# Optimization experiments

Hardware: AMD Instinct MI355X
Metric: run time of the kernel (lower is better)

## Reference

```python
import jax, jax.numpy as jnp
import numpy as np

K_SLOTS = 64
DIM = 256
HEADS = 4
DH = DIM // HEADS
EPS = 1e-20
LN_EPS = 1e-5


def layernorm(x, g, b):
    mu = jnp.mean(x, axis=-1, keepdims=True)
    var = jnp.var(x, axis=-1, keepdims=True)
    return (x - mu) * jax.lax.rsqrt(var + LN_EPS) * g + b


def setup_inputs() -> dict:
    key = jax.random.key(0)
    ks = jax.random.split(key, 12)
    B, S = 4, 32768
    s = 0.02
    return {
        "X": jax.random.normal(ks[0], (B, S, DIM), dtype=jnp.float32),
        "mu": jax.random.uniform(ks[1], (1, K_SLOTS, DIM), minval=-0.2, maxval=0.2, dtype=jnp.float32),
        "ln_s_g": jnp.ones((DIM,), jnp.float32),
        "ln_s_b": jnp.zeros((DIM,), jnp.float32),
        "Wq": jax.random.normal(ks[2], (DIM, DIM), jnp.float32) * s,
        "bq": jax.random.normal(ks[3], (DIM,), jnp.float32) * s,
        "Wk": jax.random.normal(ks[4], (DIM, DIM), jnp.float32) * s,
        "bk": jax.random.normal(ks[5], (DIM,), jnp.float32) * s,
        "Wv": jax.random.normal(ks[6], (DIM, DIM), jnp.float32) * s,
        "bv": jax.random.normal(ks[7], (DIM,), jnp.float32) * s,
        "ln_a_g": jnp.ones((DIM,), jnp.float32),
        "ln_a_b": jnp.zeros((DIM,), jnp.float32),
    }


def reference(X, mu, ln_s_g, ln_s_b, Wq, bq, Wk, bk, Wv, bv, ln_a_g, ln_a_b):
    B, S, D = X.shape
    # slots (eval mode: mu is used directly), LN then q projection
    Sq = layernorm(mu, ln_s_g, ln_s_b) @ Wq + bq            # [1, K, D]
    Q = Sq.reshape(K_SLOTS, HEADS, DH)                       # [K, H, dh] (shared over batch)
    Kp = (X @ Wk + bk).reshape(B, S, HEADS, DH)              # [B, S, H, dh]
    V = (X @ Wv + bv).reshape(B, S, HEADS, DH)
    scale = 1.0 / np.sqrt(DH).astype(np.float32)
    # scores [B, H, K, S]
    W = jnp.einsum("khd,bshd->bhks", Q, Kp) * scale
    # softmax over SLOT axis (k), then sum-normalize over sequence axis (s)
    W = jax.nn.softmax(W, axis=2)
    C = jnp.sum(W, axis=-1, keepdims=True)                   # [B, H, K, 1]
    A = W / (C + EPS)
    S_hat = jnp.einsum("bhks,bshd->bkhd", A, V).reshape(B, K_SLOTS, D)
    return layernorm(S_hat, ln_a_g, ln_a_b)
```

## Files before the change

### kernel.cpp

```cpp
#include <hip/hip_runtime.h>
#include <hip/hip_bf16.h>

#define DIM   256
#define DH    64
#define NKS   64
#define NH    4
#define SEQ   32768
#define NCOPY 8

typedef float f32x4  __attribute__((ext_vector_type(4)));
typedef short bf16x8 __attribute__((ext_vector_type(8)));

__device__ __forceinline__ unsigned short f2bf(float f) {
    union { __hip_bfloat16 b; unsigned short u; } v;
    v.b = __float2bfloat16(f);
    return v.u;
}
__device__ __forceinline__ unsigned int f2bf2(float lo, float hi) {
    return (unsigned int)f2bf(lo) | ((unsigned int)f2bf(hi) << 16);
}

__global__ void k_q(const float* __restrict__ mu, const float* __restrict__ g,
                    const float* __restrict__ bb, const float* __restrict__ Wq,
                    const float* __restrict__ bq, float* __restrict__ Q) {
    __shared__ float nrm[DIM];
    __shared__ float red1[4], red2[4];
    const int k = blockIdx.x, t = threadIdx.x;
    float x = mu[k * DIM + t];
    float s = x;
    #pragma unroll
    for (int o = 1; o <= 32; o <<= 1) s += __shfl_xor(s, o);
    if ((t & 63) == 0) red1[t >> 6] = s;
    __syncthreads();
    const float mean = (red1[0] + red1[1] + red1[2] + red1[3]) * (1.0f / DIM);
    const float d = x - mean;
    float vs = d * d;
    #pragma unroll
    for (int o = 1; o <= 32; o <<= 1) vs += __shfl_xor(vs, o);
    if ((t & 63) == 0) red2[t >> 6] = vs;
    __syncthreads();
    const float var = (red2[0] + red2[1] + red2[2] + red2[3]) * (1.0f / DIM);
    nrm[t] = d * rsqrtf(var + 1e-5f) * g[t] + bb[t];
    __syncthreads();
    float acc = bq[t];
    for (int c = 0; c < DIM; ++c) acc += nrm[c] * Wq[c * DIM + t];
    Q[k * DIM + t] = acc;
}

__global__ void k_fold(const float* __restrict__ Q, const float* __restrict__ Wk,
                       const float* __restrict__ bk, const float* __restrict__ Wv,
                       const float* __restrict__ bv,
                       unsigned short* __restrict__ W2T, float* __restrict__ b2) {
    const int n = blockIdx.x, t = threadIdx.x;
    __shared__ float q[DH];
    if (n < 256) {
        const int h = n >> 6, k = n & 63;
        if (t < DH) q[t] = Q[k * DIM + h * DH + t];
        __syncthreads();
        float acc = 0.f;
        #pragma unroll 8
        for (int d0 = 0; d0 < DH; ++d0) acc += Wk[t * DIM + h * DH + d0] * q[d0];
        W2T[n * 256 + t] = f2bf(acc * 0.125f);
        if (t == 0) {
            float ba = 0.f;
            for (int d0 = 0; d0 < DH; ++d0) ba += bk[h * DH + d0] * q[d0];
            b2[n] = ba * 0.125f;
        }
    } else {
        const int col = n - 256;
        W2T[n * 256 + t] = f2bf(Wv[t * DIM + col]);
        if (t == 0) b2[n] = bv[col];
    }
}

__global__ __launch_bounds__(1024)
void k_main_part(const float* __restrict__ X, const unsigned short* __restrict__ W2T,
                 const float* __restrict__ b2, float* __restrict__ num_p,
                 float* __restrict__ den_p) {
    extern __shared__ __align__(16) unsigned char smem[];
    const int AB = 32768, VB = 49152, SB = 65536;
    const int tid  = threadIdx.x;
    const int lane = tid & 63;
    const int wid  = tid >> 6;
    const int l15  = lane & 15;
    const int lhi  = lane >> 4;
    const int bid   = blockIdx.x;
    const int b     = bid >> 6;
    const int chunk = bid & 63;
    const float* Xg = X + ((size_t)(b * SEQ + chunk * 512)) * DIM;

    const bool is_score = wid < 8;
    const int h_sc  = wid >> 1;
    const int sh    = wid & 1;
    const int vg    = wid - 8;
    const int h_v   = vg >> 1;
    const int nbase = wid * 32;
    const int hp = wid >> 2;
    const int dq = wid & 3;

    bf16x8 bfr[8][2];
    #pragma unroll
    for (int ks = 0; ks < 8; ++ks)
        #pragma unroll
        for (int ni = 0; ni < 2; ++ni)
            bfr[ks][ni] = *(const bf16x8*)(W2T + (size_t)(nbase + ni * 16 + l15) * 256
                                           + ks * 32 + lhi * 8);
    float bias[2];
    #pragma unroll
    for (int ni = 0; ni < 2; ++ni) bias[ni] = b2[nbase + ni * 16 + l15];

    f32x4 pv[4];
    #pragma unroll
    for (int i = 0; i < 4; ++i) pv[i] = (f32x4){0.f, 0.f, 0.f, 0.f};
    float den_acc[2] = {0.f, 0.f};

    float4 pf[2];
    #pragma unroll
    for (int j = 0; j < 2; ++j) {
        const int f = j * 1024 + tid;
        pf[j] = *(const float4*)(Xg + (f >> 6) * DIM + (f & 63) * 4);
    }
    #pragma unroll
    for (int j = 0; j < 2; ++j) {
        const int f = j * 1024 + tid;
        const int row = f >> 6, c4 = f & 63;
        const int byte = row * 512 + ((c4 * 8) ^ ((row & 7) << 4));
        *(uint2*)(smem + byte) = make_uint2(f2bf2(pf[j].x, pf[j].y), f2bf2(pf[j].z, pf[j].w));
    }
    __syncthreads();

    for (int t = 0; t < 16; ++t) {
        const int tb = t & 1;
        const unsigned char* xbuf = smem + tb * 16384;

        if (t < 15) {
            const float* Xt = Xg + (size_t)(t + 1) * 32 * DIM;
            #pragma unroll
            for (int j = 0; j < 2; ++j) {
                const int f = j * 1024 + tid;
                pf[j] = *(const float4*)(Xt + (f >> 6) * DIM + (f & 63) * 4);
            }
        }

        f32x4 acc[2][2];
        #pragma unroll
        for (int si = 0; si < 2; ++si)
            #pragma unroll
            for (int ni = 0; ni < 2; ++ni)
                acc[si][ni] = (f32x4){bias[ni], bias[ni], bias[ni], bias[ni]};
        #pragma unroll
        for (int ks = 0; ks < 8; ++ks) {
            #pragma unroll
            for (int si = 0; si < 2; ++si) {
                const int row  = si * 16 + l15;
                const int byte = row * 512 + ((ks * 64 + lhi * 16) ^ ((row & 7) << 4));
                const bf16x8 afr = *(const bf16x8*)(xbuf + byte);
                #pragma unroll
                for (int ni = 0; ni < 2; ++ni)
                    acc[si][ni] = __builtin_amdgcn_mfma_f32_16x16x32_bf16(
                        afr, bfr[ks][ni], acc[si][ni], 0, 0, 0);
            }
        }

        if (is_score) {
            #pragma unroll
            for (int si = 0; si < 2; ++si) {
                #pragma unroll
                for (int ni = 0; ni < 2; ++ni)
                    #pragma unroll
                    for (int r = 0; r < 4; ++r)
                        acc[si][ni][r] = __expf(acc[si][ni][r]);
                #pragma unroll
                for (int r = 0; r < 4; ++r) {
                    float p = acc[si][0][r] + acc[si][1][r];
                    p += __shfl_xor(p, 1);
                    p += __shfl_xor(p, 2);
                    p += __shfl_xor(p, 4);
                    p += __shfl_xor(p, 8);
                    if (l15 == 0)
                        *(float*)(smem + SB + (((tb * 4 + h_sc) * 2 + sh) * 32
                                               + si * 16 + lhi * 4 + r) * 4) = p;
                }
            }
        }

        __syncthreads();

        {
            const int hh = is_score ? h_sc : h_v;
            #pragma unroll
            for (int si = 0; si < 2; ++si) {
                const int sbase = SB + ((tb * 4 + hh) * 2) * 128 + (si * 16 + lhi * 4) * 4;
                const f32x4 s0 = *(const f32x4*)(smem + sbase);
                const f32x4 s1 = *(const f32x4*)(smem + sbase + 128);
                float sinv[4];
                #pragma unroll
                for (int r = 0; r < 4; ++r) sinv[r] = 1.0f / (s0[r] + s1[r]);
                if (is_score) {
                    #pragma unroll
                    for (int ni = 0; ni < 2; ++ni) {
                        den_acc[ni] += acc[si][ni][0] * sinv[0] + acc[si][ni][1] * sinv[1]
                                     + acc[si][ni][2] * sinv[2] + acc[si][ni][3] * sinv[3];
                        const int k = sh * 32 + ni * 16 + l15;
                        const int byte = AB + (h_sc * 64 + k) * 64
                                       + ((si * 32 + lhi * 8) ^ (((k >> 1) & 3) << 4));
                        *(uint2*)(smem + byte) = make_uint2(
                            f2bf2(acc[si][ni][0], acc[si][ni][1]),
                            f2bf2(acc[si][ni][2], acc[si][ni][3]));
                    }
                } else {
                    #pragma unroll
                    for (int ni = 0; ni < 2; ++ni) {
                        const int d = vg * 32 + ni * 16 + l15;
                        const int byte = VB + d * 64
                                       + ((si * 32 + lhi * 8) ^ (((d >> 1) & 3) << 4));
                        *(uint2*)(smem + byte) = make_uint2(
                            f2bf2(acc[si][ni][0] * sinv[0], acc[si][ni][1] * sinv[1]),
                            f2bf2(acc[si][ni][2] * sinv[2], acc[si][ni][3] * sinv[3]));
                    }
                }
            }
        }
        if (t < 15) {
            unsigned char* nbuf = smem + (tb ^ 1) * 16384;
            #pragma unroll
            for (int j = 0; j < 2; ++j) {
                const int f = j * 1024 + tid;
                const int row = f >> 6, c4 = f & 63;
                const int byte = row * 512 + ((c4 * 8) ^ ((row & 7) << 4));
                *(uint2*)(nbuf + byte) = make_uint2(f2bf2(pf[j].x, pf[j].y),
                                                    f2bf2(pf[j].z, pf[j].w));
            }
        }

        __syncthreads();

        {
            bf16x8 afr[4];
            #pragma unroll
            for (int mi = 0; mi < 4; ++mi) {
                const int k = mi * 16 + l15;
                afr[mi] = *(const bf16x8*)(smem + AB + (hp * 64 + k) * 64
                                           + ((lhi * 16) ^ (((k >> 1) & 3) << 4)));
            }
            const int d = hp * 64 + dq * 16 + l15;
            const bf16x8 vfr = *(const bf16x8*)(smem + VB + d * 64
                                                + ((lhi * 16) ^ (((d >> 1) & 3) << 4)));
            #pragma unroll
            for (int mi = 0; mi < 4; ++mi)
                pv[mi] = __builtin_amdgcn_mfma_f32_16x16x32_bf16(afr[mi], vfr, pv[mi], 0, 0, 0);
        }
    }

    float* np = num_p + (size_t)bid * 16384 + hp * 4096;
    #pragma unroll
    for (int mi = 0; mi < 4; ++mi)
        #pragma unroll
        for (int r = 0; r < 4; ++r)
            np[(mi * 16 + lhi * 4 + r) * 64 + dq * 16 + l15] = pv[mi][r];
    if (is_score) {
        #pragma unroll
        for (int ni = 0; ni < 2; ++ni) {
            float v = den_acc[ni];
            v += __shfl_xor(v, 16);
            v += __shfl_xor(v, 32);
            if (lhi == 0)
                den_p[(size_t)bid * 256 + h_sc * 64 + sh * 32 + ni * 16 + l15] = v;
        }
    }
}

__global__ __launch_bounds__(1024)
void k_main_atom(const float* __restrict__ X, const unsigned short* __restrict__ W2T,
                 const float* __restrict__ b2, float* __restrict__ num_c,
                 float* __restrict__ den_c) {
    extern __shared__ __align__(16) unsigned char smem[];
    const int AB = 32768, VB = 49152, SB = 65536;
    const int tid  = threadIdx.x;
    const int lane = tid & 63;
    const int wid  = tid >> 6;
    const int l15  = lane & 15;
    const int lhi  = lane >> 4;
    const int b     = blockIdx.x >> 7;
    const int chunk = blockIdx.x & 127;
    const int copy  = blockIdx.x & (NCOPY - 1);
    const float* Xg = X + ((size_t)(b * SEQ + chunk * 256)) * DIM;

    const bool is_score = wid < 8;
    const int h_sc  = wid >> 1;
    const int sh    = wid & 1;
    const int vg    = wid - 8;
    const int h_v   = vg >> 1;
    const int nbase = wid * 32;
    const int hp = wid >> 2;
    const int dq = wid & 3;

    bf16x8 bfr[8][2];
    #pragma unroll
    for (int ks = 0; ks < 8; ++ks)
        #pragma unroll
        for (int ni = 0; ni < 2; ++ni)
            bfr[ks][ni] = *(const bf16x8*)(W2T + (size_t)(nbase + ni * 16 + l15) * 256
                                           + ks * 32 + lhi * 8);
    float bias[2];
    #pragma unroll
    for (int ni = 0; ni < 2; ++ni) bias[ni] = b2[nbase + ni * 16 + l15];

    f32x4 pv[4];
    #pragma unroll
    for (int i = 0; i < 4; ++i) pv[i] = (f32x4){0.f, 0.f, 0.f, 0.f};
    float den_acc[2] = {0.f, 0.f};

    float4 pf[2];
    #pragma unroll
    for (int j = 0; j < 2; ++j) {
        const int f = j * 1024 + tid;
        pf[j] = *(const float4*)(Xg + (f >> 6) * DIM + (f & 63) * 4);
    }
    #pragma unroll
    for (int j = 0; j < 2; ++j) {
        const int f = j * 1024 + tid;
        const int row = f >> 6, c4 = f & 63;
        const int byte = row * 512 + ((c4 * 8) ^ ((row & 7) << 4));
        *(uint2*)(smem + byte) = make_uint2(f2bf2(pf[j].x, pf[j].y), f2bf2(pf[j].z, pf[j].w));
    }
    __syncthreads();

    for (int t = 0; t < 8; ++t) {
        const int tb = t & 1;
        const unsigned char* xbuf = smem + tb * 16384;
        if (t < 7) {
            const float* Xt = Xg + (size_t)(t + 1) * 32 * DIM;
            #pragma unroll
            for (int j = 0; j < 2; ++j) {
                const int f = j * 1024 + tid;
                pf[j] = *(const float4*)(Xt + (f >> 6) * DIM + (f & 63) * 4);
            }
        }
        f32x4 acc[2][2];
        #pragma unroll
        for (int si = 0; si < 2; ++si)
            #pragma unroll
            for (int ni = 0; ni < 2; ++ni)
                acc[si][ni] = (f32x4){bias[ni], bias[ni], bias[ni], bias[ni]};
        #pragma unroll
        for (int ks = 0; ks < 8; ++ks) {
            #pragma unroll
            for (int si = 0; si < 2; ++si) {
                const int row  = si * 16 + l15;
                const int byte = row * 512 + ((ks * 64 + lhi * 16) ^ ((row & 7) << 4));
                const bf16x8 afr = *(const bf16x8*)(xbuf + byte);
                #pragma unroll
                for (int ni = 0; ni < 2; ++ni)
                    acc[si][ni] = __builtin_amdgcn_mfma_f32_16x16x32_bf16(
                        afr, bfr[ks][ni], acc[si][ni], 0, 0, 0);
            }
        }
        if (is_score) {
            #pragma unroll
            for (int si = 0; si < 2; ++si) {
                #pragma unroll
                for (int ni = 0; ni < 2; ++ni)
                    #pragma unroll
                    for (int r = 0; r < 4; ++r)
                        acc[si][ni][r] = __expf(acc[si][ni][r]);
                #pragma unroll
                for (int r = 0; r < 4; ++r) {
                    float p = acc[si][0][r] + acc[si][1][r];
                    p += __shfl_xor(p, 1);
                    p += __shfl_xor(p, 2);
                    p += __shfl_xor(p, 4);
                    p += __shfl_xor(p, 8);
                    if (l15 == 0)
                        *(float*)(smem + SB + (((tb * 4 + h_sc) * 2 + sh) * 32
                                               + si * 16 + lhi * 4 + r) * 4) = p;
                }
            }
        }
        __syncthreads();
        {
            const int hh = is_score ? h_sc : h_v;
            #pragma unroll
            for (int si = 0; si < 2; ++si) {
                const int sbase = SB + ((tb * 4 + hh) * 2) * 128 + (si * 16 + lhi * 4) * 4;
                const f32x4 s0 = *(const f32x4*)(smem + sbase);
                const f32x4 s1 = *(const f32x4*)(smem + sbase + 128);
                float sinv[4];
                #pragma unroll
                for (int r = 0; r < 4; ++r) sinv[r] = 1.0f / (s0[r] + s1[r]);
                if (is_score) {
                    #pragma unroll
                    for (int ni = 0; ni < 2; ++ni) {
                        den_acc[ni] += acc[si][ni][0] * sinv[0] + acc[si][ni][1] * sinv[1]
                                     + acc[si][ni][2] * sinv[2] + acc[si][ni][3] * sinv[3];
                        const int k = sh * 32 + ni * 16 + l15;
                        const int byte = AB + (h_sc * 64 + k) * 64
                                       + ((si * 32 + lhi * 8) ^ (((k >> 1) & 3) << 4));
                        *(uint2*)(smem + byte) = make_uint2(
                            f2bf2(acc[si][ni][0], acc[si][ni][1]),
                            f2bf2(acc[si][ni][2], acc[si][ni][3]));
                    }
                } else {
                    #pragma unroll
                    for (int ni = 0; ni < 2; ++ni) {
                        const int d = vg * 32 + ni * 16 + l15;
                        const int byte = VB + d * 64
                                       + ((si * 32 + lhi * 8) ^ (((d >> 1) & 3) << 4));
                        *(uint2*)(smem + byte) = make_uint2(
                            f2bf2(acc[si][ni][0] * sinv[0], acc[si][ni][1] * sinv[1]),
                            f2bf2(acc[si][ni][2] * sinv[2], acc[si][ni][3] * sinv[3]));
                    }
                }
            }
        }
        if (t < 7) {
            unsigned char* nbuf = smem + (tb ^ 1) * 16384;
            #pragma unroll
            for (int j = 0; j < 2; ++j) {
                const int f = j * 1024 + tid;
                const int row = f >> 6, c4 = f & 63;
                const int byte = row * 512 + ((c4 * 8) ^ ((row & 7) << 4));
                *(uint2*)(nbuf + byte) = make_uint2(f2bf2(pf[j].x, pf[j].y),
                                                    f2bf2(pf[j].z, pf[j].w));
            }
        }
        __syncthreads();
        {
            bf16x8 afr[4];
            #pragma unroll
            for (int mi = 0; mi < 4; ++mi) {
                const int k = mi * 16 + l15;
                afr[mi] = *(const bf16x8*)(smem + AB + (hp * 64 + k) * 64
                                           + ((lhi * 16) ^ (((k >> 1) & 3) << 4)));
            }
            const int d = hp * 64 + dq * 16 + l15;
            const bf16x8 vfr = *(const bf16x8*)(smem + VB + d * 64
                                                + ((lhi * 16) ^ (((d >> 1) & 3) << 4)));
            #pragma unroll
            for (int mi = 0; mi < 4; ++mi)
                pv[mi] = __builtin_amdgcn_mfma_f32_16x16x32_bf16(afr[mi], vfr, pv[mi], 0, 0, 0);
        }
    }

    if (is_score) {
        #pragma unroll
        for (int ni = 0; ni < 2; ++ni) {
            float v = den_acc[ni];
            v += __shfl_xor(v, 16);
            v += __shfl_xor(v, 32);
            if (lhi == 0)
                atomicAdd(&den_c[((copy * 4 + b) * NH + h_sc) * NKS
                                 + sh * 32 + ni * 16 + l15], v);
        }
    }
    #pragma unroll
    for (int mi = 0; mi < 4; ++mi)
        #pragma unroll
        for (int r = 0; r < 4; ++r) {
            const int k = mi * 16 + lhi * 4 + r;
            const int d = dq * 16 + l15;
            atomicAdd(&num_c[(((size_t)(copy * 4 + b) * NH + hp) * NKS + k) * DH + d],
                      pv[mi][r]);
        }
}

__global__ void k_final_part(const float* __restrict__ num_p, const float* __restrict__ den_p,
                             const float* __restrict__ ga, const float* __restrict__ gb,
                             float* __restrict__ out) {
    __shared__ float red1[4], red2[4];
    const int b = blockIdx.x >> 6, k = blockIdx.x & 63;
    const int t = threadIdx.x;
    const int h = t >> 6, dd = t & 63;
    float nsum = 0.f, dsum = 0.f;
    #pragma unroll 8
    for (int c = 0; c < 64; ++c) {
        const size_t bid = (size_t)(b * 64 + c);
        nsum += num_p[bid * 16384 + h * 4096 + k * 64 + dd];
        dsum += den_p[bid * 256 + h * 64 + k];
    }
    const float val = nsum / (dsum + 1e-20f);
    float s = val;
    #pragma unroll
    for (int o = 1; o <= 32; o <<= 1) s += __shfl_xor(s, o);
    if ((t & 63) == 0) red1[t >> 6] = s;
    __syncthreads();
    const float mean = (red1[0] + red1[1] + red1[2] + red1[3]) * (1.0f / DIM);
    const float d = val - mean;
    float vs = d * d;
    #pragma unroll
    for (int o = 1; o <= 32; o <<= 1) vs += __shfl_xor(vs, o);
    if ((t & 63) == 0) red2[t >> 6] = vs;
    __syncthreads();
    const float var = (red2[0] + red2[1] + red2[2] + red2[3]) * (1.0f / DIM);
    out[(size_t)(b * NKS + k) * DIM + t] = d * rsqrtf(var + 1e-5f) * ga[t] + gb[t];
}

__global__ void k_final_atom(const float* __restrict__ num_c, const float* __restrict__ den_c,
                             const float* __restrict__ ga, const float* __restrict__ gb,
                             float* __restrict__ out) {
    __shared__ float red1[4], red2[4];
    const int b = blockIdx.x >> 6, k = blockIdx.x & 63;
    const int t = threadIdx.x;
    const int h = t >> 6, dd = t & 63;
    float nsum = 0.f, dsum = 0.f;
    #pragma unroll
    for (int c = 0; c < NCOPY; ++c) {
        nsum += num_c[(((size_t)(c * 4 + b) * NH + h) * NKS + k) * DH + dd];
        dsum += den_c[((c * 4 + b) * NH + h) * NKS + k];
    }
    const float val = nsum / (dsum + 1e-20f);
    float s = val;
    #pragma unroll
    for (int o = 1; o <= 32; o <<= 1) s += __shfl_xor(s, o);
    if ((t & 63) == 0) red1[t >> 6] = s;
    __syncthreads();
    const float mean = (red1[0] + red1[1] + red1[2] + red1[3]) * (1.0f / DIM);
    const float d = val - mean;
    float vs = d * d;
    #pragma unroll
    for (int o = 1; o <= 32; o <<= 1) vs += __shfl_xor(vs, o);
    if ((t & 63) == 0) red2[t >> 6] = vs;
    __syncthreads();
    const float var = (red2[0] + red2[1] + red2[2] + red2[3]) * (1.0f / DIM);
    out[(size_t)(b * NKS + k) * DIM + t] = d * rsqrtf(var + 1e-5f) * ga[t] + gb[t];
}

extern "C" void kernel_launch(void* const* d_in, const int* in_sizes, int n_in,
                              void* d_out, int out_size, void* d_ws, size_t ws_size,
                              hipStream_t stream) {
    const float* X      = (const float*)d_in[0];
    const float* mu     = (const float*)d_in[1];
    const float* ln_s_g = (const float*)d_in[2];
    const float* ln_s_b = (const float*)d_in[3];
    const float* Wq     = (const float*)d_in[4];
    const float* bq     = (const float*)d_in[5];
    const float* Wk     = (const float*)d_in[6];
    const float* bk     = (const float*)d_in[7];
    const float* Wv     = (const float*)d_in[8];
    const float* bv     = (const float*)d_in[9];
    const float* ln_a_g = (const float*)d_in[10];
    const float* ln_a_b = (const float*)d_in[11];
    float* out = (float*)d_out;

    char* ws = (char*)d_ws;
    float*          Q     = (float*)(ws);
    unsigned short* W2T   = (unsigned short*)(ws + 65536);
    float*          b2    = (float*)(ws + 327680);

    hipFuncSetAttribute((const void*)k_main_part,
                        hipFuncAttributeMaxDynamicSharedMemorySize, 67584);
    hipFuncSetAttribute((const void*)k_main_atom,
                        hipFuncAttributeMaxDynamicSharedMemorySize, 67584);
    hipLaunchKernelGGL(k_q,    dim3(64),  dim3(256), 0, stream, mu, ln_s_g, ln_s_b, Wq, bq, Q);
    hipLaunchKernelGGL(k_fold, dim3(512), dim3(256), 0, stream, Q, Wk, bk, Wv, bv, W2T, b2);

    const size_t need = 329728 + (size_t)256 * 16384 * 4 + (size_t)256 * 256 * 4;
    if (ws_size >= need) {
        float* num_p = (float*)(ws + 329728);
        float* den_p = (float*)(ws + 329728 + 16777216);
        hipLaunchKernelGGL(k_main_part, dim3(256), dim3(1024), 67584, stream,
                           X, W2T, b2, num_p, den_p);
        hipLaunchKernelGGL(k_final_part, dim3(256), dim3(256), 0, stream,
                           num_p, den_p, ln_a_g, ln_a_b, out);
    } else {
        float* num_c = (float*)(ws + 329728);
        float* den_c = (float*)(ws + 2426880);
        hipMemsetAsync(ws + 329728, 0, 2097152 + 32768, stream);
        hipLaunchKernelGGL(k_main_atom, dim3(512), dim3(1024), 67584, stream,
                           X, W2T, b2, num_c, den_c);
        hipLaunchKernelGGL(k_final_atom, dim3(256), dim3(256), 0, stream,
                           num_c, den_c, ln_a_g, ln_a_b, out);
    }
}
```

Measured before the change: 150.3 us.

## Split fused attention-pooling kernel into separate weight and PV passes

Replaces the single fused kernel (score warps plus value warps in 1024-thread blocks) with two kernels. The first computes slot-softmaxed weights and writes them to global memory in bf16, together with partial denominators. The second recomputes V from X and multiplies it by the stored weights. A final kernel reduces 128 partials per batch and applies layernorm. The aim is smaller blocks and better per-kernel occupancy, at the cost of reading X twice and a large global round-trip for the weight matrix. The atomic fallback path is removed.

```diff
diff --git a/kernel.cpp b/kernel.cpp
--- a/kernel.cpp
+++ b/kernel.cpp
@@ -6,7 +6,6 @@
 #define NKS   64
 #define NH    4
 #define SEQ   32768
-#define NCOPY 8
 
 typedef float f32x4  __attribute__((ext_vector_type(4)));
 typedef short bf16x8 __attribute__((ext_vector_type(8)));
@@ -73,6 +72,342 @@
     }
 }
 
+__global__ __launch_bounds__(512)
+void k_w(const float* __restrict__ X, const unsigned short* __restrict__ W2T,
+         const float* __restrict__ b2, unsigned short* __restrict__ WT,
+         float* __restrict__ den_p) {
+    extern __shared__ __align__(16) unsigned char smem[];
+    const int SB = 32768;
+    const int tid  = threadIdx.x;
+    const int lane = tid & 63;
+    const int wid  = tid >> 6;
+    const int l15  = lane & 15;
+    const int lhi  = lane >> 4;
+    const int bid   = blockIdx.x;
+    const int b     = bid >> 7;
+    const int chunk = bid & 127;
+    const float* Xg = X + ((size_t)(b * SEQ + chunk * 256)) * DIM;
+
+    const int h  = wid >> 1;
+    const int sh = wid & 1;
+    const int nbase = wid * 32;
+
+    bf16x8 bfr[8][2];
+    #pragma unroll
+    for (int ks = 0; ks < 8; ++ks)
+        #pragma unroll
+        for (int ni = 0; ni < 2; ++ni)
+            bfr[ks][ni] = *(const bf16x8*)(W2T + (size_t)(nbase + ni * 16 + l15) * 256
+                                           + ks * 32 + lhi * 8);
+    float bias[2];
+    #pragma unroll
+    for (int ni = 0; ni < 2; ++ni) bias[ni] = b2[nbase + ni * 16 + l15];
+
+    float den_acc[2] = {0.f, 0.f};
+
+    float4 pf[4];
+    #pragma unroll
+    for (int j = 0; j < 4; ++j) {
+        const int f = j * 512 + tid;
+        pf[j] = *(const float4*)(Xg + (f >> 6) * DIM + (f & 63) * 4);
+    }
+    #pragma unroll
+    for (int j = 0; j < 4; ++j) {
+        const int f = j * 512 + tid;
+        const int row = f >> 6, c4 = f & 63;
+        const int byte = row * 512 + ((c4 * 8) ^ ((row & 7) << 4));
+        *(uint2*)(smem + byte) = make_uint2(f2bf2(pf[j].x, pf[j].y), f2bf2(pf[j].z, pf[j].w));
+    }
+    __syncthreads();
+
+    for (int t = 0; t < 8; ++t) {
+        const int tb = t & 1;
+        const unsigned char* xbuf = smem + tb * 16384;
+
+        if (t < 7) {
+            const float* Xt = Xg + (size_t)(t + 1) * 32 * DIM;
+            #pragma unroll
+            for (int j = 0; j < 4; ++j) {
+                const int f = j * 512 + tid;
+                pf[j] = *(const float4*)(Xt + (f >> 6) * DIM + (f & 63) * 4);
+            }
+        }
+
+        f32x4 acc[2][2];
+        #pragma unroll
+        for (int si = 0; si < 2; ++si)
+            #pragma unroll
+            for (int ni = 0; ni < 2; ++ni)
+                acc[si][ni] = (f32x4){bias[ni], bias[ni], bias[ni], bias[ni]};
+        #pragma unroll
+        for (int ks = 0; ks < 8; ++ks) {
+            #pragma unroll
+            for (int si = 0; si < 2; ++si) {
+                const int row  = si * 16 + l15;
+                const int byte = row * 512 + ((ks * 64 + lhi * 16) ^ ((row & 7) << 4));
+                const bf16x8 afr = *(const bf16x8*)(xbuf + byte);
+                #pragma unroll
+                for (int ni = 0; ni < 2; ++ni)
+                    acc[si][ni] = __builtin_amdgcn_mfma_f32_16x16x32_bf16(
+                        afr, bfr[ks][ni], acc[si][ni], 0, 0, 0);
+            }
+        }
+
+        #pragma unroll
+        for (int si = 0; si < 2; ++si) {
+            #pragma unroll
+            for (int ni = 0; ni < 2; ++ni)
+                #pragma unroll
+                for (int r = 0; r < 4; ++r)
+                    acc[si][ni][r] = __expf(acc[si][ni][r]);
+            #pragma unroll
+            for (int r = 0; r < 4; ++r) {
+                float p = acc[si][0][r] + acc[si][1][r];
+                p += __shfl_xor(p, 1);
+                p += __shfl_xor(p, 2);
+                p += __shfl_xor(p, 4);
+                p += __shfl_xor(p, 8);
+                if (l15 == 0)
+                    *(float*)(smem + SB + (((tb * 4 + h) * 2 + sh) * 32
+                                           + si * 16 + lhi * 4 + r) * 4) = p;
+            }
+        }
+        __syncthreads();
+
+        const int srow = chunk * 256 + t * 32;
+        #pragma unroll
+        for (int si = 0; si < 2; ++si) {
+            const int sbase = SB + ((tb * 4 + h) * 2) * 128 + (si * 16 + lhi * 4) * 4;
+            const f32x4 s0 = *(const f32x4*)(smem + sbase);
+            const f32x4 s1 = *(const f32x4*)(smem + sbase + 128);
+            float sinv[4];
+            #pragma unroll
+            for (int r = 0; r < 4; ++r) sinv[r] = 1.0f / (s0[r] + s1[r]);
+            #pragma unroll
+            for (int ni = 0; ni < 2; ++ni) {
+                const float w0 = acc[si][ni][0] * sinv[0], w1 = acc[si][ni][1] * sinv[1];
+                const float w2 = acc[si][ni][2] * sinv[2], w3 = acc[si][ni][3] * sinv[3];
+                den_acc[ni] += (w0 + w1) + (w2 + w3);
+                const size_t row = (size_t)((b * 4 + h) * 64 + sh * 32 + ni * 16 + l15);
+                *(uint2*)(WT + row * SEQ + srow + si * 16 + lhi * 4) =
+                    make_uint2(f2bf2(w0, w1), f2bf2(w2, w3));
+            }
+        }
+        if (t < 7) {
+            unsigned char* nbuf = smem + (tb ^ 1) * 16384;
+            #pragma unroll
+            for (int j = 0; j < 4; ++j) {
+                const int f = j * 512 + tid;
+                const int row = f >> 6, c4 = f & 63;
+                const int byte = row * 512 + ((c4 * 8) ^ ((row & 7) << 4));
+                *(uint2*)(nbuf + byte) = make_uint2(f2bf2(pf[j].x, pf[j].y),
+                                                    f2bf2(pf[j].z, pf[j].w));
+            }
+        }
+        __syncthreads();
+    }
+
+    #pragma unroll
+    for (int ni = 0; ni < 2; ++ni) {
+        float v = den_acc[ni];
+        v += __shfl_xor(v, 16);
+        v += __shfl_xor(v, 32);
+        if (lhi == 0)
+            den_p[(size_t)bid * 256 + wid * 32 + ni * 16 + l15] = v;
+    }
+}
+
+__global__ __launch_bounds__(512)
+void k_pv(const float* __restrict__ X, const unsigned short* __restrict__ W2T,
+          const float* __restrict__ b2, const unsigned short* __restrict__ WT,
+          float* __restrict__ num_p) {
+    extern __shared__ __align__(16) unsigned char smem[];
+    const int VB = 16384;
+    const int tid  = threadIdx.x;
+    const int lane = tid & 63;
+    const int wid  = tid >> 6;
+    const int l15  = lane & 15;
+    const int lhi  = lane >> 4;
+    const int bid   = blockIdx.x;
+    const int b     = bid >> 7;
+    const int chunk = bid & 127;
+    const float* Xg = X + ((size_t)(b * SEQ + chunk * 256)) * DIM;
+
+    const int h  = wid >> 1;
+    const int kh = wid & 1;
+    const int vbase = 256 + wid * 32;
+
+    bf16x8 bfr_lo[4][2];
+    #pragma unroll
+    for (int ks = 0; ks < 4; ++ks)
+        #pragma unroll
+        for (int nj = 0; nj < 2; ++nj)
+            bfr_lo[ks][nj] = *(const bf16x8*)(W2T + (size_t)(vbase + nj * 16 + l15) * 256
+                                              + ks * 32 + lhi * 8);
+    float bias[2];
+    #pragma unroll
+    for (int nj = 0; nj < 2; ++nj) bias[nj] = b2[vbase + nj * 16 + l15];
+
+    f32x4 pv[2][4];
+    #pragma unroll
+    for (int mi = 0; mi < 2; ++mi)
+        #pragma unroll
+        for (int nj = 0; nj < 4; ++nj) pv[mi][nj] = (f32x4){0.f, 0.f, 0.f, 0.f};
+
+    bf16x8 af[2];
+    float4 pf[2];
+    #pragma unroll
+    for (int j = 0; j < 2; ++j) {
+        const int f = j * 512 + tid;
+        pf[j] = *(const float4*)(Xg + (f >> 6) * DIM + (f & 63) * 4);
+    }
+    #pragma unroll
+    for (int j = 0; j < 2; ++j) {
+        const int f = j * 512 + tid;
+        const int row = f >> 6, c4 = f & 63;
+        const int byte = row * 512 + ((c4 * 8) ^ ((row & 7) << 4));
+        *(uint2*)(smem + byte) = make_uint2(f2bf2(pf[j].x, pf[j].y), f2bf2(pf[j].z, pf[j].w));
+    }
+    __syncthreads();
+
+    for (int t = 0; t < 16; ++t) {
+        const int P = t >> 1, half = t & 1, tb = t & 1, vb = P & 1;
+        const unsigned char* xbuf = smem + tb * 8192;
+
+        if (half == 0 && P > 0) {
+            bf16x8 vB[4];
+            #pragma unroll
+            for (int nj = 0; nj < 4; ++nj) {
+                const int c = h * 64 + nj * 16 + l15;
+                vB[nj] = *(const bf16x8*)(smem + VB + (vb ^ 1) * 16384 + c * 64
+                                          + ((lhi * 16) ^ (((c >> 1) & 3) << 4)));
+            }
+            #pragma unroll
+            for (int mi = 0; mi < 2; ++mi)
+                #pragma unroll
+                for (int nj = 0; nj < 4; ++nj)
+                    pv[mi][nj] = __builtin_amdgcn_mfma_f32_16x16x32_bf16(
+                        af[mi], vB[nj], pv[mi][nj], 0, 0, 0);
+        }
+        if (half == 0) {
+            const int s0 = chunk * 256 + P * 32 + lhi * 8;
+            #pragma unroll
+            for (int mi = 0; mi < 2; ++mi) {
+                const size_t row = (size_t)((b * 4 + h) * 64 + kh * 32 + mi * 16 + l15);
+                af[mi] = *(const bf16x8*)(WT + row * SEQ + s0);
+            }
+        }
+        if (t < 15) {
+            const float* Xt = Xg + (size_t)(t + 1) * 16 * DIM;
+            #pragma unroll
+            for (int j = 0; j < 2; ++j) {
+                const int f = j * 512 + tid;
+                pf[j] = *(const float4*)(Xt + (f >> 6) * DIM + (f & 63) * 4);
+            }
+        }
+
+        bf16x8 bh[4][2];
+        #pragma unroll
+        for (int ks = 0; ks < 4; ++ks)
+            #pragma unroll
+            for (int nj = 0; nj < 2; ++nj)
+                bh[ks][nj] = *(const bf16x8*)(W2T + (size_t)(vbase + nj * 16 + l15) * 256
+                                              + (ks + 4) * 32 + lhi * 8);
+        f32x4 vacc[2];
+        #pragma unroll
+        for (int nj = 0; nj < 2; ++nj)
+            vacc[nj] = (f32x4){bias[nj], bias[nj], bias[nj], bias[nj]};
+        #pragma unroll
+        for (int ks = 0; ks < 8; ++ks) {
+            const int byte = l15 * 512 + ((ks * 64 + lhi * 16) ^ ((l15 & 7) << 4));
+            const bf16x8 afr = *(const bf16x8*)(xbuf + byte);
+            #pragma unroll
+            for (int nj = 0; nj < 2; ++nj)
+                vacc[nj] = __builtin_amdgcn_mfma_f32_16x16x32_bf16(
+                    afr, ks < 4 ? bfr_lo[ks][nj] : bh[ks - 4][nj], vacc[nj], 0, 0, 0);
+        }
+        __syncthreads();
+
+        #pragma unroll
+        for (int nj = 0; nj < 2; ++nj) {
+            const int c = wid * 32 + nj * 16 + l15;
+            const int byte = VB + vb * 16384 + c * 64
+                           + ((half * 32 + lhi * 8) ^ (((c >> 1) & 3) << 4));
+            *(uint2*)(smem + byte) = make_uint2(f2bf2(vacc[nj][0], vacc[nj][1]),
+                                                f2bf2(vacc[nj][2], vacc[nj][3]));
+        }
+        if (t < 15) {
+            unsigned char* nbuf = smem + (tb ^ 1) * 8192;
+            #pragma unroll
+            for (int j = 0; j < 2; ++j) {
+                const int f = j * 512 + tid;
+                const int row = f >> 6, c4 = f & 63;
+                const int byte = row * 512 + ((c4 * 8) ^ ((row & 7) << 4));
+                *(uint2*)(nbuf + byte) = make_uint2(f2bf2(pf[j].x, pf[j].y),
+                                                    f2bf2(pf[j].z, pf[j].w));
+            }
+        }
+        __syncthreads();
+    }
+
+    {
+        bf16x8 vB[4];
+        #pragma unroll
+        for (int nj = 0; nj < 4; ++nj) {
+            const int c = h * 64 + nj * 16 + l15;
+            vB[nj] = *(const bf16x8*)(smem + VB + 16384 + c * 64
+                                      + ((lhi * 16) ^ (((c >> 1) & 3) << 4)));
+        }
+        #pragma unroll
+        for (int mi = 0; mi < 2; ++mi)
+            #pragma unroll
+            for (int nj = 0; nj < 4; ++nj)
+                pv[mi][nj] = __builtin_amdgcn_mfma_f32_16x16x32_bf16(
+                    af[mi], vB[nj], pv[mi][nj], 0, 0, 0);
+    }
+
+    #pragma unroll
+    for (int mi = 0; mi < 2; ++mi)
+        #pragma unroll
+        for (int nj = 0; nj < 4; ++nj)
+            #pragma unroll
+            for (int r = 0; r < 4; ++r) {
+                const int k = kh * 32 + mi * 16 + lhi * 4 + r;
+                num_p[(((size_t)bid * 4 + h) * 64 + k) * 64 + nj * 16 + l15] = pv[mi][nj][r];
+            }
+}
+
+__global__ void k_final2(const float* __restrict__ num_p, const float* __restrict__ den_p,
+                         const float* __restrict__ ga, const float* __restrict__ gb,
+                         float* __restrict__ out) {
+    __shared__ float red1[4], red2[4];
+    const int b = blockIdx.x >> 6, k = blockIdx.x & 63;
+    const int t = threadIdx.x;
+    const int h = t >> 6, dd = t & 63;
+    float nsum = 0.f, dsum = 0.f;
+    #pragma unroll 8
+    for (int c = 0; c < 128; ++c) {
+        const size_t bid = (size_t)(b * 128 + c);
+        nsum += num_p[((bid * 4 + h) * 64 + k) * 64 + dd];
+        dsum += den_p[bid * 256 + h * 64 + k];
+    }
+    const float val = nsum / (dsum + 1e-20f);
+    float s = val;
+    #pragma unroll
+    for (int o = 1; o <= 32; o <<= 1) s += __shfl_xor(s, o);
+    if ((t & 63) == 0) red1[t >> 6] = s;
+    __syncthreads();
+    const float mean = (red1[0] + red1[1] + red1[2] + red1[3]) * (1.0f / DIM);
+    const float d = val - mean;
+    float vs = d * d;
+    #pragma unroll
+    for (int o = 1; o <= 32; o <<= 1) vs += __shfl_xor(vs, o);
+    if ((t & 63) == 0) red2[t >> 6] = vs;
+    __syncthreads();
+    const float var = (red2[0] + red2[1] + red2[2] + red2[3]) * (1.0f / DIM);
+    out[(size_t)(b * NKS + k) * DIM + t] = d * rsqrtf(var + 1e-5f) * ga[t] + gb[t];
+}
+
 __global__ __launch_bounds__(1024)
 void k_main_part(const float* __restrict__ X, const unsigned short* __restrict__ W2T,
                  const float* __restrict__ b2, float* __restrict__ num_p,
@@ -88,7 +423,6 @@
     const int b     = bid >> 6;
     const int chunk = bid & 63;
     const float* Xg = X + ((size_t)(b * SEQ + chunk * 512)) * DIM;
-
     const bool is_score = wid < 8;
     const int h_sc  = wid >> 1;
     const int sh    = wid & 1;
@@ -97,7 +431,6 @@
     const int nbase = wid * 32;
     const int hp = wid >> 2;
     const int dq = wid & 3;
-
     bf16x8 bfr[8][2];
     #pragma unroll
     for (int ks = 0; ks < 8; ++ks)
@@ -108,12 +441,10 @@
     float bias[2];
     #pragma unroll
     for (int ni = 0; ni < 2; ++ni) bias[ni] = b2[nbase + ni * 16 + l15];
-
     f32x4 pv[4];
     #pragma unroll
     for (int i = 0; i < 4; ++i) pv[i] = (f32x4){0.f, 0.f, 0.f, 0.f};
     float den_acc[2] = {0.f, 0.f};
-
     float4 pf[2];
     #pragma unroll
     for (int j = 0; j < 2; ++j) {
@@ -128,11 +459,9 @@
         *(uint2*)(smem + byte) = make_uint2(f2bf2(pf[j].x, pf[j].y), f2bf2(pf[j].z, pf[j].w));
     }
     __syncthreads();
-
     for (int t = 0; t < 16; ++t) {
         const int tb = t & 1;
         const unsigned char* xbuf = smem + tb * 16384;
-
         if (t < 15) {
             const float* Xt = Xg + (size_t)(t + 1) * 32 * DIM;
             #pragma unroll
@@ -141,7 +470,6 @@
                 pf[j] = *(const float4*)(Xt + (f >> 6) * DIM + (f & 63) * 4);
             }
         }
-
         f32x4 acc[2][2];
         #pragma unroll
         for (int si = 0; si < 2; ++si)
@@ -161,7 +489,6 @@
                         afr, bfr[ks][ni], acc[si][ni], 0, 0, 0);
             }
         }
-
         if (is_score) {
             #pragma unroll
             for (int si = 0; si < 2; ++si) {
@@ -183,9 +510,7 @@
                 }
             }
         }
-
         __syncthreads();
-
         {
             const int hh = is_score ? h_sc : h_v;
             #pragma unroll
@@ -232,9 +557,7 @@
                                                     f2bf2(pf[j].z, pf[j].w));
             }
         }
-
         __syncthreads();
-
         {
             bf16x8 afr[4];
             #pragma unroll
@@ -251,7 +574,6 @@
                 pv[mi] = __builtin_amdgcn_mfma_f32_16x16x32_bf16(afr[mi], vfr, pv[mi], 0, 0, 0);
         }
     }
-
     float* np = num_p + (size_t)bid * 16384 + hp * 4096;
     #pragma unroll
     for (int mi = 0; mi < 4; ++mi)
@@ -268,200 +590,6 @@
                 den_p[(size_t)bid * 256 + h_sc * 64 + sh * 32 + ni * 16 + l15] = v;
         }
     }
-}
-
-__global__ __launch_bounds__(1024)
-void k_main_atom(const float* __restrict__ X, const unsigned short* __restrict__ W2T,
-                 const float* __restrict__ b2, float* __restrict__ num_c,
-                 float* __restrict__ den_c) {
-    extern __shared__ __align__(16) unsigned char smem[];
-    const int AB = 32768, VB = 49152, SB = 65536;
-    const int tid  = threadIdx.x;
-    const int lane = tid & 63;
-    const int wid  = tid >> 6;
-    const int l15  = lane & 15;
-    const int lhi  = lane >> 4;
-    const int b     = blockIdx.x >> 7;
-    const int chunk = blockIdx.x & 127;
-    const int copy  = blockIdx.x & (NCOPY - 1);
-    const float* Xg = X + ((size_t)(b * SEQ + chunk * 256)) * DIM;
-
-    const bool is_score = wid < 8;
-    const int h_sc  = wid >> 1;
-    const int sh    = wid & 1;
-    const int vg    = wid - 8;
-    const int h_v   = vg >> 1;
-    const int nbase = wid * 32;
-    const int hp = wid >> 2;
-    const int dq = wid & 3;
-
-    bf16x8 bfr[8][2];
-    #pragma unroll
-    for (int ks = 0; ks < 8; ++ks)
-        #pragma unroll
-        for (int ni = 0; ni < 2; ++ni)
-            bfr[ks][ni] = *(const bf16x8*)(W2T + (size_t)(nbase + ni * 16 + l15) * 256
-                                           + ks * 32 + lhi * 8);
-    float bias[2];
-    #pragma unroll
-    for (int ni = 0; ni < 2; ++ni) bias[ni] = b2[nbase + ni * 16 + l15];
-
-    f32x4 pv[4];
-    #pragma unroll
-    for (int i = 0; i < 4; ++i) pv[i] = (f32x4){0.f, 0.f, 0.f, 0.f};
-    float den_acc[2] = {0.f, 0.f};
-
-    float4 pf[2];
-    #pragma unroll
-    for (int j = 0; j < 2; ++j) {
-        const int f = j * 1024 + tid;
-        pf[j] = *(const float4*)(Xg + (f >> 6) * DIM + (f & 63) * 4);
-    }
-    #pragma unroll
-    for (int j = 0; j < 2; ++j) {
-        const int f = j * 1024 + tid;
-        const int row = f >> 6, c4 = f & 63;
-        const int byte = row * 512 + ((c4 * 8) ^ ((row & 7) << 4));
-        *(uint2*)(smem + byte) = make_uint2(f2bf2(pf[j].x, pf[j].y), f2bf2(pf[j].z, pf[j].w));
-    }
-    __syncthreads();
-
-    for (int t = 0; t < 8; ++t) {
-        const int tb = t & 1;
-        const unsigned char* xbuf = smem + tb * 16384;
-        if (t < 7) {
-            const float* Xt = Xg + (size_t)(t + 1) * 32 * DIM;
-            #pragma unroll
-            for (int j = 0; j < 2; ++j) {
-                const int f = j * 1024 + tid;
-                pf[j] = *(const float4*)(Xt + (f >> 6) * DIM + (f & 63) * 4);
-            }
-        }
-        f32x4 acc[2][2];
-        #pragma unroll
-        for (int si = 0; si < 2; ++si)
-            #pragma unroll
-            for (int ni = 0; ni < 2; ++ni)
-                acc[si][ni] = (f32x4){bias[ni], bias[ni], bias[ni], bias[ni]};
-        #pragma unroll
-        for (int ks = 0; ks < 8; ++ks) {
-            #pragma unroll
-            for (int si = 0; si < 2; ++si) {
-                const int row  = si * 16 + l15;
-                const int byte = row * 512 + ((ks * 64 + lhi * 16) ^ ((row & 7) << 4));
-                const bf16x8 afr = *(const bf16x8*)(xbuf + byte);
-                #pragma unroll
-                for (int ni = 0; ni < 2; ++ni)
-                    acc[si][ni] = __builtin_amdgcn_mfma_f32_16x16x32_bf16(
-                        afr, bfr[ks][ni], acc[si][ni], 0, 0, 0);
-            }
-        }
-        if (is_score) {
-            #pragma unroll
-            for (int si = 0; si < 2; ++si) {
-                #pragma unroll
-                for (int ni = 0; ni < 2; ++ni)
-                    #pragma unroll
-                    for (int r = 0; r < 4; ++r)
-                        acc[si][ni][r] = __expf(acc[si][ni][r]);
-                #pragma unroll
-                for (int r = 0; r < 4; ++r) {
-                    float p = acc[si][0][r] + acc[si][1][r];
-                    p += __shfl_xor(p, 1);
-                    p += __shfl_xor(p, 2);
-                    p += __shfl_xor(p, 4);
-                    p += __shfl_xor(p, 8);
-                    if (l15 == 0)
-                        *(float*)(smem + SB + (((tb * 4 + h_sc) * 2 + sh) * 32
-                                               + si * 16 + lhi * 4 + r) * 4) = p;
-                }
-            }
-        }
-        __syncthreads();
-        {
-            const int hh = is_score ? h_sc : h_v;
-            #pragma unroll
-            for (int si = 0; si < 2; ++si) {
-                const int sbase = SB + ((tb * 4 + hh) * 2) * 128 + (si * 16 + lhi * 4) * 4;
-                const f32x4 s0 = *(const f32x4*)(smem + sbase);
-                const f32x4 s1 = *(const f32x4*)(smem + sbase + 128);
-                float sinv[4];
-                #pragma unroll
-                for (int r = 0; r < 4; ++r) sinv[r] = 1.0f / (s0[r] + s1[r]);
-                if (is_score) {
-                    #pragma unroll
-                    for (int ni = 0; ni < 2; ++ni) {
-                        den_acc[ni] += acc[si][ni][0] * sinv[0] + acc[si][ni][1] * sinv[1]
-                                     + acc[si][ni][2] * sinv[2] + acc[si][ni][3] * sinv[3];
-                        const int k = sh * 32 + ni * 16 + l15;
-                        const int byte = AB + (h_sc * 64 + k) * 64
-                                       + ((si * 32 + lhi * 8) ^ (((k >> 1) & 3) << 4));
-                        *(uint2*)(smem + byte) = make_uint2(
-                            f2bf2(acc[si][ni][0], acc[si][ni][1]),
-                            f2bf2(acc[si][ni][2], acc[si][ni][3]));
-                    }
-                } else {
-                    #pragma unroll
-                    for (int ni = 0; ni < 2; ++ni) {
-                        const int d = vg * 32 + ni * 16 + l15;
-                        const int byte = VB + d * 64
-                                       + ((si * 32 + lhi * 8) ^ (((d >> 1) & 3) << 4));
-                        *(uint2*)(smem + byte) = make_uint2(
-                            f2bf2(acc[si][ni][0] * sinv[0], acc[si][ni][1] * sinv[1]),
-                            f2bf2(acc[si][ni][2] * sinv[2], acc[si][ni][3] * sinv[3]));
-                    }
-                }
-            }
-        }
-        if (t < 7) {
-            unsigned char* nbuf = smem + (tb ^ 1) * 16384;
-            #pragma unroll
-            for (int j = 0; j < 2; ++j) {
-                const int f = j * 1024 + tid;
-                const int row = f >> 6, c4 = f & 63;
-                const int byte = row * 512 + ((c4 * 8) ^ ((row & 7) << 4));
-                *(uint2*)(nbuf + byte) = make_uint2(f2bf2(pf[j].x, pf[j].y),
-                                                    f2bf2(pf[j].z, pf[j].w));
-            }
-        }
-        __syncthreads();
-        {
-            bf16x8 afr[4];
-            #pragma unroll
-            for (int mi = 0; mi < 4; ++mi) {
-                const int k = mi * 16 + l15;
-                afr[mi] = *(const bf16x8*)(smem + AB + (hp * 64 + k) * 64
-                                           + ((lhi * 16) ^ (((k >> 1) & 3) << 4)));
-            }
-            const int d = hp * 64 + dq * 16 + l15;
-            const bf16x8 vfr = *(const bf16x8*)(smem + VB + d * 64
-                                                + ((lhi * 16) ^ (((d >> 1) & 3) << 4)));
-            #pragma unroll
-            for (int mi = 0; mi < 4; ++mi)
-                pv[mi] = __builtin_amdgcn_mfma_f32_16x16x32_bf16(afr[mi], vfr, pv[mi], 0, 0, 0);
-        }
-    }
-
-    if (is_score) {
-        #pragma unroll
-        for (int ni = 0; ni < 2; ++ni) {
-            float v = den_acc[ni];
-            v += __shfl_xor(v, 16);
-            v += __shfl_xor(v, 32);
-            if (lhi == 0)
-                atomicAdd(&den_c[((copy * 4 + b) * NH + h_sc) * NKS
-                                 + sh * 32 + ni * 16 + l15], v);
-        }
-    }
-    #pragma unroll
-    for (int mi = 0; mi < 4; ++mi)
-        #pragma unroll
-        for (int r = 0; r < 4; ++r) {
-            const int k = mi * 16 + lhi * 4 + r;
-            const int d = dq * 16 + l15;
-            atomicAdd(&num_c[(((size_t)(copy * 4 + b) * NH + hp) * NKS + k) * DH + d],
-                      pv[mi][r]);
-        }
 }
 
 __global__ void k_final_part(const float* __restrict__ num_p, const float* __restrict__ den_p,
@@ -477,36 +605,6 @@
         const size_t bid = (size_t)(b * 64 + c);
         nsum += num_p[bid * 16384 + h * 4096 + k * 64 + dd];
         dsum += den_p[bid * 256 + h * 64 + k];
-    }
-    const float val = nsum / (dsum + 1e-20f);
-    float s = val;
-    #pragma unroll
-    for (int o = 1; o <= 32; o <<= 1) s += __shfl_xor(s, o);
-    if ((t & 63) == 0) red1[t >> 6] = s;
-    __syncthreads();
-    const float mean = (red1[0] + red1[1] + red1[2] + red1[3]) * (1.0f / DIM);
-    const float d = val - mean;
-    float vs = d * d;
-    #pragma unroll
-    for (int o = 1; o <= 32; o <<= 1) vs += __shfl_xor(vs, o);
-    if ((t & 63) == 0) red2[t >> 6] = vs;
-    __syncthreads();
-    const float var = (red2[0] + red2[1] + red2[2] + red2[3]) * (1.0f / DIM);
-    out[(size_t)(b * NKS + k) * DIM + t] = d * rsqrtf(var + 1e-5f) * ga[t] + gb[t];
-}
-
-__global__ void k_final_atom(const float* __restrict__ num_c, const float* __restrict__ den_c,
-                             const float* __restrict__ ga, const float* __restrict__ gb,
-                             float* __restrict__ out) {
-    __shared__ float red1[4], red2[4];
-    const int b = blockIdx.x >> 6, k = blockIdx.x & 63;
-    const int t = threadIdx.x;
-    const int h = t >> 6, dd = t & 63;
-    float nsum = 0.f, dsum = 0.f;
-    #pragma unroll
-    for (int c = 0; c < NCOPY; ++c) {
-        nsum += num_c[(((size_t)(c * 4 + b) * NH + h) * NKS + k) * DH + dd];
-        dsum += den_c[((c * 4 + b) * NH + h) * NKS + k];
     }
     const float val = nsum / (dsum + 1e-20f);
     float s = val;
@@ -543,32 +641,34 @@
     float* out = (float*)d_out;
 
     char* ws = (char*)d_ws;
-    float*          Q     = (float*)(ws);
-    unsigned short* W2T   = (unsigned short*)(ws + 65536);
-    float*          b2    = (float*)(ws + 327680);
-
-    hipFuncSetAttribute((const void*)k_main_part,
-                        hipFuncAttributeMaxDynamicSharedMemorySize, 67584);
-    hipFuncSetAttribute((const void*)k_main_atom,
-                        hipFuncAttributeMaxDynamicSharedMemorySize, 67584);
+    float*          Q   = (float*)(ws);
+    unsigned short* W2T = (unsigned short*)(ws + 65536);
+    float*          b2  = (float*)(ws + 327680);
+
     hipLaunchKernelGGL(k_q,    dim3(64),  dim3(256), 0, stream, mu, ln_s_g, ln_s_b, Wq, bq, Q);
     hipLaunchKernelGGL(k_fold, dim3(512), dim3(256), 0, stream, Q, Wk, bk, Wv, bv, W2T, b2);
 
-    const size_t need = 329728 + (size_t)256 * 16384 * 4 + (size_t)256 * 256 * 4;
-    if (ws_size >= need) {
+    const size_t WT_OFF  = 329728;
+    const size_t NUM_OFF = WT_OFF + (size_t)1024 * SEQ * 2;
+    const size_t DEN_OFF = NUM_OFF + (size_t)512 * 16384 * 4;
+    const size_t need2   = DEN_OFF + (size_t)512 * 256 * 4;
+
+    if (ws_size >= need2) {
+        unsigned short* WT    = (unsigned short*)(ws + WT_OFF);
+        float*          num_p = (float*)(ws + NUM_OFF);
+        float*          den_p = (float*)(ws + DEN_OFF);
+        hipLaunchKernelGGL(k_w,  dim3(512), dim3(512), 34816, stream, X, W2T, b2, WT, den_p);
+        hipLaunchKernelGGL(k_pv, dim3(512), dim3(512), 49152, stream, X, W2T, b2, WT, num_p);
+        hipLaunchKernelGGL(k_final2, dim3(256), dim3(256), 0, stream,
+                           num_p, den_p, ln_a_g, ln_a_b, out);
+    } else {
         float* num_p = (float*)(ws + 329728);
         float* den_p = (float*)(ws + 329728 + 16777216);
+        hipFuncSetAttribute((const void*)k_main_part,
+                            hipFuncAttributeMaxDynamicSharedMemorySize, 67584);
         hipLaunchKernelGGL(k_main_part, dim3(256), dim3(1024), 67584, stream,
                            X, W2T, b2, num_p, den_p);
         hipLaunchKernelGGL(k_final_part, dim3(256), dim3(256), 0, stream,
                            num_p, den_p, ln_a_g, ln_a_b, out);
-    } else {
-        float* num_c = (float*)(ws + 329728);
-        float* den_c = (float*)(ws + 2426880);
-        hipMemsetAsync(ws + 329728, 0, 2097152 + 32768, stream);
-        hipLaunchKernelGGL(k_main_atom, dim3(512), dim3(1024), 67584, stream,
-                           X, W2T, b2, num_c, den_c);
-        hipLaunchKernelGGL(k_final_atom, dim3(256), dim3(256), 0, stream,
-                           num_c, den_c, ln_a_g, ln_a_b, out);
-    }
-}
+    }
+}
```

Measured after the change: 130.2 us. -13.4%, faster.
